# Kernel tuning notes

Hardware: AMD Instinct MI355X
Metric: run time of the kernel (lower is better)

Reference implementation:

```python
import jax, jax.numpy as jnp
import numpy as np

H, D, R, S, K, EV = 8, 256, 6, 2, 2, 2   # num_heads, head_dim, ratio, shared_head, topk, expand_v
HID = 2048
DV = D * EV            # head_v_dim = 512
KEY_DIM = H * D        # 2048
VAL_DIM = KEY_DIM * EV # 4096


def setup_inputs() -> dict:
    key = jax.random.key(0)
    ks = jax.random.split(key, 9)
    b, t = 2, 1024
    def lin(k, fan_in, shape):
        # ~torch default linear init scale
        return jax.random.normal(k, shape, jnp.float32) * (fan_in ** -0.5)
    return {
        "hidden_states": jax.random.normal(ks[0], (b, t, HID), jnp.float32),
        "Wq": lin(ks[1], HID, (HID, KEY_DIM)),
        "Wk": lin(ks[2], HID, (HID, KEY_DIM)),
        "Wv": lin(ks[3], HID, (HID, VAL_DIM)),
        "Wq_exp": lin(ks[4], D, (H, D, D * R)),  # per-head q expert expansion (ModuleList -> batched)
        "Wk_exp": lin(ks[5], D, (H, D, D * R)),
        "Wgate": lin(ks[6], D, (D, R - S)),
        "Wg": lin(ks[7], HID, (HID, VAL_DIM)),
        "Wo": lin(ks[8], VAL_DIM, (VAL_DIM, HID)),
    }


def reference(hidden_states, Wq, Wk, Wv, Wq_exp, Wk_exp, Wgate, Wg, Wo):
    b, t, _ = hidden_states.shape
    # base projections, split into heads: [H, b, t, D]
    q = (hidden_states @ Wq).reshape(b, t, H, D).transpose(2, 0, 1, 3)
    k = (hidden_states @ Wk).reshape(b, t, H, D).transpose(2, 0, 1, 3)
    v = (hidden_states @ Wv).reshape(b, t, H, DV)  # [b, t, H, DV]

    # --- sparse routing on q (gate over ratio - shared experts) ---
    logits = jnp.einsum('hbtd,dn->hbtn', q, Wgate)
    scores = jax.nn.softmax(logits.astype(jnp.float32), axis=-1)
    w, idx = jax.lax.top_k(scores, K)
    w = w / jnp.sum(w, axis=-1, keepdims=True)
    idx = idx + S  # shift past shared experts
    # scatter top-k weights into full [H, b, t, R]
    full = jnp.sum(jax.nn.one_hot(idx, R, dtype=w.dtype) * w[..., None], axis=-2)
    full = full.at[..., :S].set(1.0 / S)
    full = full / jnp.sum(full, axis=-1, keepdims=True)
    rw = full.astype(hidden_states.dtype).transpose(3, 1, 2, 0)  # [R, b, t, H]
    mask = (rw != 0).astype(hidden_states.dtype)                 # [R, b, t, H]

    # --- per-head expert expansions: [R, b, t, H, D] ---
    qe = jnp.einsum('hbtd,hde->hbte', q, Wq_exp).reshape(H, b, t, R, D).transpose(3, 1, 2, 0, 4)
    ke = jnp.einsum('hbtd,hde->hbte', k, Wk_exp).reshape(H, b, t, R, D).transpose(3, 1, 2, 0, 4)
    ve = jnp.broadcast_to(v[None], (R, b, t, H, DV))
    qe = qe * mask[..., None]
    ke = ke * mask[..., None]
    ve = ve * mask[..., None]

    # --- dense attention per (expert, batch, head) ---
    attn = jax.nn.softmax(jnp.einsum('rbqhd,rbkhd->rbhqk', qe, ke) / (D ** 0.5), axis=-1)
    o = jnp.einsum('rbhqk,rbkhd->rbqhd', attn, ve)  # [R, b, t, H, DV]

    # --- weighted combine over experts + gated output ---
    o = jnp.einsum('rbthd,rbth->bthd', o, rw)
    g = (hidden_states @ Wg).reshape(b, t, H, DV)
    o = o * jax.nn.silu(g)
    return o.reshape(b, t, VAL_DIM) @ Wo
```

## Files before the change

kernel.cpp:

```cpp
#include <hip/hip_runtime.h>
#include <hip/hip_bf16.h>
#include <cstdint>
#include <cstddef>

typedef __bf16 bf16_t;
typedef __bf16 bf16x8 __attribute__((ext_vector_type(8)));
typedef float f32x4 __attribute__((ext_vector_type(4)));

typedef __attribute__((address_space(3))) unsigned int lds_uint_t;
typedef __attribute__((address_space(1))) unsigned int glob_uint_t;

__device__ __forceinline__ void gload16(const void* g, void* l) {
  __builtin_amdgcn_global_load_lds((const glob_uint_t*)g, (lds_uint_t*)l, 16, 0, 0);
}

__device__ __forceinline__ f32x4 mfma16(bf16x8 a, bf16x8 b, f32x4 c) {
  return __builtin_amdgcn_mfma_f32_16x16x32_bf16(a, b, c, 0, 0, 0);
}

__global__ __launch_bounds__(256) void conv_bf16_k(const float* __restrict__ in,
                                                   bf16_t* __restrict__ out, int n8) {
  int i = blockIdx.x * 256 + threadIdx.x;
  if (i >= n8) return;
  f32x4 a = *(const f32x4*)(in + (size_t)i * 8);
  f32x4 b = *(const f32x4*)(in + (size_t)i * 8 + 4);
  bf16x8 o;
  o[0] = (bf16_t)a[0]; o[1] = (bf16_t)a[1]; o[2] = (bf16_t)a[2]; o[3] = (bf16_t)a[3];
  o[4] = (bf16_t)b[0]; o[5] = (bf16_t)b[1]; o[6] = (bf16_t)b[2]; o[7] = (bf16_t)b[3];
  *(bf16x8*)(out + (size_t)i * 8) = o;
}

__global__ __launch_bounds__(256) void tconv_k(const float* __restrict__ in, bf16_t* __restrict__ out,
                                               int R, int C, size_t inZ, size_t outZ) {
  __shared__ __align__(16) bf16_t t[64 * 72];
  in += (size_t)blockIdx.z * inZ;
  out += (size_t)blockIdx.z * outZ;
  const int c0 = blockIdx.x * 64, r0 = blockIdx.y * 64;
  const int tid = threadIdx.x;
#pragma unroll
  for (int it = 0; it < 4; it++) {
    int c = tid + it * 256;
    int row = c >> 4, ch = c & 15;
    f32x4 v = *(const f32x4*)(in + (size_t)(r0 + row) * C + c0 + ch * 4);
#pragma unroll
    for (int j = 0; j < 4; j++) t[(ch * 4 + j) * 72 + row] = (bf16_t)v[j];
  }
  __syncthreads();
#pragma unroll
  for (int it = 0; it < 2; it++) {
    int c = tid + it * 256;
    int oc = c >> 3, ch = c & 7;
    bf16x8 v = *(const bf16x8*)(t + oc * 72 + ch * 8);
    *(bf16x8*)(out + (size_t)(c0 + oc) * R + r0 + ch * 8) = v;
  }
}

__global__ __launch_bounds__(256) void tv_k(const bf16_t* __restrict__ v, bf16_t* __restrict__ Vt) {
  __shared__ __align__(16) bf16_t t[64 * 72];
  const int tt0 = blockIdx.x * 64;
  const int dv0 = blockIdx.y * 64;
  const int bh = blockIdx.z;
  const int b = bh >> 3, h = bh & 7;
  const int tid = threadIdx.x;
  const bf16_t* src = v + (size_t)(b * 1024 + tt0) * 12288 + 8192 + h * 512 + dv0;
#pragma unroll
  for (int it = 0; it < 2; it++) {
    int c = tid + it * 256;
    int row = c >> 3, ch = c & 7;
    bf16x8 x = *(const bf16x8*)(src + (size_t)row * 12288 + ch * 8);
#pragma unroll
    for (int j = 0; j < 8; j++) t[(ch * 8 + j) * 72 + row] = x[j];
  }
  __syncthreads();
  bf16_t* dst = Vt + (size_t)bh * 524288 + (size_t)dv0 * 1024 + tt0;
#pragma unroll
  for (int it = 0; it < 2; it++) {
    int c = tid + it * 256;
    int od = c >> 3, ch = c & 7;
    bf16x8 x = *(const bf16x8*)(t + od * 72 + ch * 8);
    *(bf16x8*)(dst + (size_t)od * 1024 + ch * 8) = x;
  }
}

__global__ __launch_bounds__(256) void wfuse_k(const float* __restrict__ Wq, const float* __restrict__ Wgate,
                                               float* __restrict__ Wf) {
  __shared__ float wg[1024];
  const int tid = threadIdx.x;
  for (int i = tid; i < 1024; i += 256) wg[i] = Wgate[i];
  __syncthreads();
  const int kk = blockIdx.x * 64 + (tid & 63);
  const int oid = tid >> 6;
  float acc[8] = {0, 0, 0, 0, 0, 0, 0, 0};
  const float* wr = Wq + (size_t)kk * 2048;
#pragma unroll
  for (int half = 0; half < 2; half++) {
    const int h = oid * 2 + half;
    const float* seg = wr + h * 256;
    for (int d = 0; d < 256; d += 4) {
      f32x4 q4 = *(const f32x4*)(seg + d);
#pragma unroll
      for (int n = 0; n < 4; n++) {
        acc[half * 4 + n] += q4[0] * wg[(d + 0) * 4 + n] + q4[1] * wg[(d + 1) * 4 + n] +
                             q4[2] * wg[(d + 2) * 4 + n] + q4[3] * wg[(d + 3) * 4 + n];
      }
    }
  }
#pragma unroll
  for (int jj = 0; jj < 8; jj++) Wf[(size_t)kk * 32 + oid * 8 + jj] = acc[jj];
}

__global__ __launch_bounds__(256) void logits_k(const float* __restrict__ hs, const float* __restrict__ Wf,
                                                float* __restrict__ lg) {
  __shared__ __align__(16) float hrow[2048];
  __shared__ float red[8][32];
  const int bt = blockIdx.x;
  const int tid = threadIdx.x;
  const float* src = hs + (size_t)bt * 2048;
  for (int i = tid; i < 512; i += 256) *(f32x4*)&hrow[i * 4] = *(const f32x4*)(src + i * 4);
  __syncthreads();
  const int j = tid & 31, part = tid >> 5;
  float acc = 0.f;
  for (int kk = part * 256; kk < part * 256 + 256; kk++) acc += hrow[kk] * Wf[(size_t)kk * 32 + j];
  red[part][j] = acc;
  __syncthreads();
  if (tid < 32) {
    float s = 0.f;
#pragma unroll
    for (int p = 0; p < 8; p++) s += red[p][tid];
    lg[(size_t)bt * 32 + tid] = s;
  }
}

__global__ __launch_bounds__(256) void routing_k(const float* __restrict__ lg, float* __restrict__ rw) {
  int gid = blockIdx.x * 256 + threadIdx.x;
  if (gid >= 16384) return;
  const int h = gid >> 11;
  const int bt = gid & 2047;
  const int b = bt >> 10, tt = bt & 1023;
  f32x4 l = *(const f32x4*)(lg + (size_t)bt * 32 + h * 4);
  float mx = fmaxf(fmaxf(l[0], l[1]), fmaxf(l[2], l[3]));
  float e0 = __expf(l[0] - mx), e1 = __expf(l[1] - mx), e2 = __expf(l[2] - mx), e3 = __expf(l[3] - mx);
  float den = e0 + e1 + e2 + e3;
  float s[4] = {e0 / den, e1 / den, e2 / den, e3 / den};
  int i1 = 0;
#pragma unroll
  for (int i = 1; i < 4; i++) if (s[i] > s[i1]) i1 = i;
  int i2 = (i1 == 0) ? 1 : 0;
#pragma unroll
  for (int i = 0; i < 4; i++) if (i != i1 && s[i] > s[i2]) i2 = i;
  float sw = s[i1] + s[i2];
  float w1 = s[i1] / sw, w2 = s[i2] / sw;
  float tot = 1.0f + w1 + w2;
  float o[6] = {0.5f / tot, 0.5f / tot, 0.f, 0.f, 0.f, 0.f};
  o[2 + i1] = w1 / tot;
  o[2 + i2] = w2 / tot;
#pragma unroll
  for (int r = 0; r < 6; r++) rw[(size_t)((r * 2 + b) * 8 + h) * 1024 + tt] = o[r];
}

__global__ __launch_bounds__(256) void idx_k(const float* __restrict__ rw, int* __restrict__ kidx,
                                             float* __restrict__ maskg, int2* __restrict__ kn) {
  __shared__ int wsum[4];
  const int z = blockIdx.x;
  const int rr = z >> 4, bh = z & 15;
  const int b = bh >> 3, h = bh & 7;
  const float* rwp = rw + (size_t)(((rr + 2) * 2 + b) * 8 + h) * 1024;
  const int tid = threadIdx.x;
  const int lane = tid & 63, wv = tid >> 6;
  int act[4];
  int c = 0;
#pragma unroll
  for (int j = 0; j < 4; j++) { act[j] = (rwp[tid * 4 + j] != 0.f) ? 1 : 0; c += act[j]; }
  int s = c;
  for (int o = 1; o < 64; o <<= 1) { int t = __shfl_up(s, o, 64); if (lane >= o) s += t; }
  if (lane == 63) wsum[wv] = s;
  __syncthreads();
  int base = 0;
  for (int wi = 0; wi < wv; wi++) base += wsum[wi];
  int excl = base + s - c;
  int Na = wsum[0] + wsum[1] + wsum[2] + wsum[3];
  int* kout = kidx + (size_t)z * 1088;
  float* mout = maskg + (size_t)z * 1088;
  int o = excl;
#pragma unroll
  for (int j = 0; j < 4; j++)
    if (act[j]) { kout[o] = tid * 4 + j; mout[o] = 1.f; o++; }
  for (int i = Na + tid; i < 1088; i += 256) { kout[i] = 0; mout[i] = 0.f; }
  if (tid == 0) kn[z] = make_int2(Na, (Na + 63) & ~63);
}

__global__ __launch_bounds__(256) void vgather_k(const bf16_t* __restrict__ qkg, const int* __restrict__ kidx,
                                                 const int2* __restrict__ kn, bf16_t* __restrict__ Vg) {
  __shared__ __align__(16) bf16_t t[64 * 72];
  __shared__ int idx[64];
  const int z = blockIdx.z;
  const int rr = z >> 4, bh = z & 15;
  const int b = bh >> 3, h = bh & 7;
  int2 k = kn[z];
  const int s0 = blockIdx.x * 64;
  if (s0 >= k.y) return;
  const int dv0 = blockIdx.y * 64;
  const int tid = threadIdx.x;
  if (tid < 64) idx[tid] = kidx[(size_t)z * 1088 + s0 + tid];
  __syncthreads();
  int base = 0;
  for (int r2 = 0; r2 < rr; r2++) base += kn[r2 * 16 + bh].y;
#pragma unroll
  for (int it = 0; it < 2; it++) {
    int cc = tid + it * 256;
    int row = cc >> 3, ch = cc & 7;
    const bf16_t* src = qkg + (size_t)(b * 1024 + idx[row]) * 12288 + 8192 + h * 512 + dv0 + ch * 8;
    bf16x8 x = *(const bf16x8*)src;
#pragma unroll
    for (int j = 0; j < 8; j++) t[(ch * 8 + j) * 72 + row] = x[j];
  }
  __syncthreads();
  bf16_t* dst = Vg + (size_t)(bh * 512 + dv0) * 2304 + base + s0;
#pragma unroll
  for (int it = 0; it < 2; it++) {
    int cc = tid + it * 256;
    int od = cc >> 3, ch = cc & 7;
    bf16x8 x = *(const bf16x8*)(t + od * 72 + ch * 8);
    *(bf16x8*)(dst + (size_t)od * 2304 + ch * 8) = x;
  }
}

template <int MODE>
__global__ __launch_bounds__(256) void gemm_bt(const bf16_t* __restrict__ A, const bf16_t* __restrict__ B,
                                               void* __restrict__ Cp, int K, int lda, int ldb, int ldc) {
  __shared__ __align__(16) bf16_t lsA[128 * 64];
  __shared__ __align__(16) bf16_t lsB[128 * 64];
  const int tid = threadIdx.x;
  const int lane = tid & 63, wv = tid >> 6;
  const int lrow = lane & 15, lgrp = lane >> 4;
  const int wr = wv >> 1, wc = wv & 1;
  const int bn = blockIdx.x * 128, bm = blockIdx.y * 128;

  f32x4 zero = {0.f, 0.f, 0.f, 0.f};
  f32x4 acc[4][4];
#pragma unroll
  for (int i = 0; i < 4; i++)
#pragma unroll
    for (int j = 0; j < 4; j++) acc[i][j] = zero;

  for (int k0 = 0; k0 < K; k0 += 64) {
    __syncthreads();
#pragma unroll
    for (int it = 0; it < 4; it++) {
      int c = tid + it * 256;
      int row = c >> 3, coff = (c & 7) * 16;
      gload16((const char*)A + ((size_t)(bm + row) * lda + k0) * 2 + coff, (char*)lsA + row * 128 + coff);
      gload16((const char*)B + ((size_t)(bn + row) * ldb + k0) * 2 + coff, (char*)lsB + row * 128 + coff);
    }
    __syncthreads();
#pragma unroll
    for (int kk = 0; kk < 2; kk++) {
      bf16x8 af[4], bfr[4];
#pragma unroll
      for (int m4 = 0; m4 < 4; m4++)
        af[m4] = *(const bf16x8*)((const char*)lsA + (wr * 64 + m4 * 16 + lrow) * 128 + kk * 64 + lgrp * 16);
#pragma unroll
      for (int n4 = 0; n4 < 4; n4++)
        bfr[n4] = *(const bf16x8*)((const char*)lsB + (wc * 64 + n4 * 16 + lrow) * 128 + kk * 64 + lgrp * 16);
#pragma unroll
      for (int m4 = 0; m4 < 4; m4++)
#pragma unroll
        for (int n4 = 0; n4 < 4; n4++) acc[m4][n4] = mfma16(af[m4], bfr[n4], acc[m4][n4]);
    }
  }
#pragma unroll
  for (int m4 = 0; m4 < 4; m4++) {
#pragma unroll
    for (int i = 0; i < 4; i++) {
      const int row = bm + wr * 64 + m4 * 16 + lgrp * 4 + i;
#pragma unroll
      for (int n4 = 0; n4 < 4; n4++) {
        const int col = bn + wc * 64 + n4 * 16 + lrow;
        float v = acc[m4][n4][i];
        if constexpr (MODE == 0) {
          ((bf16_t*)Cp)[(size_t)row * ldc + col] = (bf16_t)v;
        } else {
          ((float*)Cp)[(size_t)row * ldc + col] = v;
        }
      }
    }
  }
}

__global__ __launch_bounds__(256) void gemm_n64(const bf16_t* __restrict__ A, const bf16_t* __restrict__ B,
                                                float* __restrict__ C, int K, int lda, int ldb, int ldc) {
  __shared__ __align__(16) bf16_t lsA[128 * 64];
  __shared__ __align__(16) bf16_t lsB[64 * 64];
  const int tid = threadIdx.x;
  const int lane = tid & 63, wr = tid >> 6;
  const int lrow = lane & 15, lgrp = lane >> 4;
  const int bn = blockIdx.x * 64, bm = blockIdx.y * 128;

  f32x4 zero = {0.f, 0.f, 0.f, 0.f};
  f32x4 acc[2][4];
#pragma unroll
  for (int i = 0; i < 2; i++)
#pragma unroll
    for (int j = 0; j < 4; j++) acc[i][j] = zero;

  for (int k0 = 0; k0 < K; k0 += 64) {
    __syncthreads();
#pragma unroll
    for (int it = 0; it < 4; it++) {
      int c = tid + it * 256;
      int row = c >> 3, coff = (c & 7) * 16;
      gload16((const char*)A + ((size_t)(bm + row) * lda + k0) * 2 + coff, (char*)lsA + row * 128 + coff);
    }
#pragma unroll
    for (int it = 0; it < 2; it++) {
      int c = tid + it * 256;
      int row = c >> 3, coff = (c & 7) * 16;
      gload16((const char*)B + ((size_t)(bn + row) * ldb + k0) * 2 + coff, (char*)lsB + row * 128 + coff);
    }
    __syncthreads();
#pragma unroll
    for (int kk = 0; kk < 2; kk++) {
      bf16x8 af[2], bfr[4];
#pragma unroll
      for (int m2 = 0; m2 < 2; m2++)
        af[m2] = *(const bf16x8*)((const char*)lsA + (wr * 32 + m2 * 16 + lrow) * 128 + kk * 64 + lgrp * 16);
#pragma unroll
      for (int n4 = 0; n4 < 4; n4++)
        bfr[n4] = *(const bf16x8*)((const char*)lsB + (n4 * 16 + lrow) * 128 + kk * 64 + lgrp * 16);
#pragma unroll
      for (int m2 = 0; m2 < 2; m2++)
#pragma unroll
        for (int n4 = 0; n4 < 4; n4++) acc[m2][n4] = mfma16(af[m2], bfr[n4], acc[m2][n4]);
    }
  }
#pragma unroll
  for (int m2 = 0; m2 < 2; m2++) {
#pragma unroll
    for (int i = 0; i < 4; i++) {
      const int row = bm + wr * 32 + m2 * 16 + lgrp * 4 + i;
#pragma unroll
      for (int n4 = 0; n4 < 4; n4++) {
        C[(size_t)row * ldc + bn + n4 * 16 + lrow] = acc[m2][n4][i];
      }
    }
  }
}

__global__ __launch_bounds__(256) void gemm_exp(const bf16_t* __restrict__ qkg, const bf16_t* __restrict__ Wqe,
                                                const bf16_t* __restrict__ Wke, bf16_t* __restrict__ qeB,
                                                bf16_t* __restrict__ keB) {
  __shared__ __align__(16) bf16_t lsA[128 * 64];
  __shared__ __align__(16) bf16_t lsB[128 * 64];
  const int tid = threadIdx.x;
  const int lane = tid & 63, wv = tid >> 6;
  const int lrow = lane & 15, lgrp = lane >> 4;
  const int wr = wv >> 1, wc = wv & 1;
  const int bn = blockIdx.x * 128, bm = blockIdx.y * 128;
  const int z = blockIdx.z;
  const int sel = z >> 3, hh = z & 7;
  const bf16_t* A = qkg + sel * 2048 + hh * 256;
  const bf16_t* B = (sel ? Wke : Wqe) + (size_t)hh * 393216;
  bf16_t* C = sel ? keB : qeB;

  f32x4 zero = {0.f, 0.f, 0.f, 0.f};
  f32x4 acc[4][4];
#pragma unroll
  for (int i = 0; i < 4; i++)
#pragma unroll
    for (int j = 0; j < 4; j++) acc[i][j] = zero;

  for (int k0 = 0; k0 < 256; k0 += 64) {
    __syncthreads();
#pragma unroll
    for (int it = 0; it < 4; it++) {
      int c = tid + it * 256;
      int row = c >> 3, coff = (c & 7) * 16;
      gload16((const char*)A + ((size_t)(bm + row) * 12288 + k0) * 2 + coff, (char*)lsA + row * 128 + coff);
      gload16((const char*)B + ((size_t)(bn + row) * 256 + k0) * 2 + coff, (char*)lsB + row * 128 + coff);
    }
    __syncthreads();
#pragma unroll
    for (int kk = 0; kk < 2; kk++) {
      bf16x8 af[4], bfr[4];
#pragma unroll
      for (int m4 = 0; m4 < 4; m4++)
        af[m4] = *(const bf16x8*)((const char*)lsA + (wr * 64 + m4 * 16 + lrow) * 128 + kk * 64 + lgrp * 16);
#pragma unroll
      for (int n4 = 0; n4 < 4; n4++)
        bfr[n4] = *(const bf16x8*)((const char*)lsB + (wc * 64 + n4 * 16 + lrow) * 128 + kk * 64 + lgrp * 16);
#pragma unroll
      for (int m4 = 0; m4 < 4; m4++)
#pragma unroll
        for (int n4 = 0; n4 < 4; n4++) acc[m4][n4] = mfma16(af[m4], bfr[n4], acc[m4][n4]);
    }
  }
#pragma unroll
  for (int m4 = 0; m4 < 4; m4++) {
#pragma unroll
    for (int i = 0; i < 4; i++) {
      const int row = bm + wr * 64 + m4 * 16 + lgrp * 4 + i;
      const int bb = row >> 10, tt = row & 1023;
#pragma unroll
      for (int n4 = 0; n4 < 4; n4++) {
        const int col = bn + wc * 64 + n4 * 16 + lrow;
        const int rr = col >> 8, dd = col & 255;
        C[((size_t)((rr * 2 + bb) * 8 + hh) * 1024 + tt) * 256 + dd] = (bf16_t)acc[m4][n4][i];
      }
    }
  }
}

__global__ __launch_bounds__(256, 2) void attn_k(const bf16_t* __restrict__ qe, const bf16_t* __restrict__ ke,
                                                 const bf16_t* __restrict__ Vt, const float* __restrict__ rw,
                                                 const bf16_t* __restrict__ g, bf16_t* __restrict__ oc,
                                                 const int* __restrict__ kidx, const float* __restrict__ maskg,
                                                 const int2* __restrict__ kn, const bf16_t* __restrict__ Vg) {
  __shared__ __align__(16) bf16_t ldsK[2][32 * 256];
  __shared__ __align__(16) bf16_t ldsV[2][256 * 32];
  __shared__ __align__(16) bf16_t ldsP[4 * 16 * 40];
  __shared__ int ldsIdx[1088];

  const int f = (blockIdx.x & 7) * 64 + (blockIdx.x >> 3);
  const int qt = f & 15, dvh = (f >> 4) & 1, bh = f >> 5;

  const int tid = threadIdx.x;
  const int wv = tid >> 6, lane = tid & 63;
  const int lrow = lane & 15, lgrp = lane >> 4;
  const int b = bh >> 3, h = bh & 7;
  const int qw = qt * 64 + wv * 16;

  const char* vtb = (const char*)Vt + ((size_t)bh * 524288 + (size_t)dvh * 262144) * 2;

  f32x4 zero = {0.f, 0.f, 0.f, 0.f};
  f32x4 Otot[16];
#pragma unroll
  for (int n = 0; n < 16; n++) Otot[n] = zero;

  int cur = 0;
  for (int r = 0; r < 6; r++) {
    const size_t rbh = (size_t)((r * 2 + b) * 8 + h);
    const bf16_t* qbase = qe + rbh * 262144;
    const float* rwb = rw + rbh * 1024;
    const char* kbr = (const char*)ke + rbh * 524288;

    int nkt = 32;
    float lpinit = 0.f;
    const float* mgp = nullptr;
    const char* vgb = vtb;
    size_t vstride = 2048;
    const bool routed = (r >= 2);
    if (routed) {
      const int rr = r - 2;
      int2 kkn = kn[rr * 16 + bh];
      nkt = kkn.y >> 5;
      lpinit = (float)(1024 - kkn.x) * 0.0625f;
      int basep = 0;
      for (int r2 = 0; r2 < rr; r2++) basep += kn[r2 * 16 + bh].y;
      vgb = (const char*)Vg + ((size_t)(bh * 512 + dvh * 256) * 2304 + basep) * 2;
      vstride = 4608;
      mgp = maskg + (size_t)(rr * 16 + bh) * 1088;
      __syncthreads();
      const int* kp = kidx + (size_t)(rr * 16 + bh) * 1088;
      for (int i = tid; i < 1088; i += 256) ldsIdx[i] = kp[i];
      __syncthreads();
    }
    if (nkt == 0) continue;

    bf16x8 qf[8];
#pragma unroll
    for (int c = 0; c < 8; c++)
      qf[c] = *(const bf16x8*)(qbase + (size_t)(qw + lrow) * 256 + c * 32 + lgrp * 8);
    float rwq[4];
#pragma unroll
    for (int i = 0; i < 4; i++) rwq[i] = rwb[qw + lgrp * 4 + i];

    float Lp[4] = {lpinit, lpinit, lpinit, lpinit};
    f32x4 accO[16];
#pragma unroll
    for (int n = 0; n < 16; n++) accO[n] = zero;

    auto issue_tile = [&](int kt, int buf) {
      char* lk = (char*)ldsK[buf];
      if (!routed) {
#pragma unroll
        for (int it = 0; it < 4; it++) {
          int p = (wv * 4 + it) * 1024 + (lane << 4);
          int row = p >> 9, off = p & 511;
          gload16(kbr + (size_t)(kt * 32 + row) * 512 + (off ^ ((row & 7) << 4)), lk + p);
        }
      } else {
#pragma unroll
        for (int it = 0; it < 4; it++) {
          int p = (wv * 4 + it) * 1024 + (lane << 4);
          int row = p >> 9, off = p & 511;
          int iv = ldsIdx[kt * 32 + row];
          gload16(kbr + (size_t)iv * 512 + (off ^ ((row & 7) << 4)), lk + p);
        }
      }
      char* lv = (char*)ldsV[buf];
      const char* vb = vgb + (size_t)kt * 64;
#pragma unroll
      for (int it = 0; it < 4; it++) {
        int p = (wv * 4 + it) * 1024 + (lane << 4);
        int row = p >> 6, off = p & 63;
        gload16(vb + (size_t)row * vstride + (off ^ (((row >> 1) & 3) << 4)), lv + p);
      }
    };

    issue_tile(0, cur);
    for (int kt = 0; kt < nkt; kt++) {
      asm volatile("s_waitcnt vmcnt(0) lgkmcnt(0)" ::: "memory");
      __syncthreads();
      if (kt + 1 < nkt) issue_tile(kt + 1, cur ^ 1);
      const char* lK = (const char*)ldsK[cur];
      const char* lV = (const char*)ldsV[cur];
      float mg0 = 1.f, mg1 = 1.f;
      if (routed) { mg0 = mgp[kt * 32 + lrow]; mg1 = mgp[kt * 32 + 16 + lrow]; }

      f32x4 sac0 = zero, sac1 = zero;
      __builtin_amdgcn_s_setprio(1);
#pragma unroll
      for (int c = 0; c < 8; c++) {
        int col = (c * 64 + lgrp * 16) ^ ((lrow & 7) << 4);
        bf16x8 k0 = *(const bf16x8*)(lK + (size_t)lrow * 512 + col);
        bf16x8 k1 = *(const bf16x8*)(lK + (size_t)(16 + lrow) * 512 + col);
        sac0 = mfma16(qf[c], k0, sac0);
        sac1 = mfma16(qf[c], k1, sac1);
      }
      __builtin_amdgcn_s_setprio(0);
      bf16_t* pb = ldsP + wv * 640;
#pragma unroll
      for (int i = 0; i < 4; i++) {
        float p0 = mg0 * __expf(sac0[i] * 0.0625f);
        float p1 = mg1 * __expf(sac1[i] * 0.0625f);
        pb[(i * 4 + lgrp) * 40 + lrow] = (bf16_t)p0;
        pb[(i * 4 + lgrp) * 40 + 16 + lrow] = (bf16_t)p1;
        Lp[i] += p0 + p1;
      }
      bf16x8 pa = *(const bf16x8*)(pb + ((lrow & 3) * 4 + (lrow >> 2)) * 40 + lgrp * 8);
      __builtin_amdgcn_s_setprio(1);
#pragma unroll
      for (int n = 0; n < 16; n++) {
        int row = n * 16 + lrow;
        int col = (lgrp * 16) ^ (((row >> 1) & 3) << 4);
        bf16x8 vf = *(const bf16x8*)(lV + (size_t)row * 64 + col);
        accO[n] = mfma16(pa, vf, accO[n]);
      }
      __builtin_amdgcn_s_setprio(0);
      cur ^= 1;
    }
#pragma unroll
    for (int i = 0; i < 4; i++) {
      float v = Lp[i];
      v += __shfl_xor(v, 1, 16);
      v += __shfl_xor(v, 2, 16);
      v += __shfl_xor(v, 4, 16);
      v += __shfl_xor(v, 8, 16);
      float inv = rwq[i] / v;
#pragma unroll
      for (int n = 0; n < 16; n++) Otot[n][i] += accO[n][i] * inv;
    }
  }

#pragma unroll
  for (int i = 0; i < 4; i++) {
    const size_t grow = ((size_t)(b * 1024 + qw + lgrp * 4 + i)) * 12288 + 4096 + h * 512 + dvh * 256;
    const size_t orow = ((size_t)(b * 1024 + qw + lgrp * 4 + i)) * 4096 + h * 512 + dvh * 256;
#pragma unroll
    for (int n = 0; n < 16; n++) {
      float gv = (float)g[grow + n * 16 + lrow];
      float sg = gv / (1.f + __expf(-gv));
      oc[orow + n * 16 + lrow] = (bf16_t)(Otot[n][i] * sg);
    }
  }
}

extern "C" void kernel_launch(void* const* d_in, const int* in_sizes, int n_in,
                              void* d_out, int out_size, void* d_ws, size_t ws_size,
                              hipStream_t stream) {
  const float* hs  = (const float*)d_in[0];
  const float* Wq  = (const float*)d_in[1];
  const float* Wk  = (const float*)d_in[2];
  const float* Wv  = (const float*)d_in[3];
  const float* Wqe = (const float*)d_in[4];
  const float* Wke = (const float*)d_in[5];
  const float* Wgt = (const float*)d_in[6];
  const float* Wg  = (const float*)d_in[7];
  const float* Wo  = (const float*)d_in[8];
  float* out = (float*)d_out;

  const size_t MB = 1024 * 1024;
  char* w = (char*)d_ws;
  bf16_t* hs_bf = (bf16_t*)(w + 0 * MB);
  bf16_t* WcatT = (bf16_t*)(w + 8 * MB);
  bf16_t* qeB   = (bf16_t*)(w + 0 * MB);
  bf16_t* WoT   = (bf16_t*)(w + 56 * MB);
  bf16_t* WqeT  = (bf16_t*)(w + 72 * MB);
  bf16_t* WkeT  = (bf16_t*)(w + 78 * MB);
  bf16_t* qkg   = (bf16_t*)(w + 84 * MB);
  bf16_t* Vt    = (bf16_t*)(w + 132 * MB);
  bf16_t* keB   = (bf16_t*)(w + 148 * MB);
  bf16_t* ocB   = (bf16_t*)(w + 196 * MB);
  float*  Wf    = (float*)(w + 212 * MB);
  float*  lg    = (float*)(w + 212 * MB + 262144);
  float*  rwB   = (float*)(w + 212 * MB + 524288);
  bf16_t* VgB   = (bf16_t*)(w + 214 * MB);
  int*    kidxB = (int*)(w + 250 * MB);
  float*  maskgB= (float*)(w + 250 * MB + 524288);
  int2*   knB   = (int2*)(w + 250 * MB + 1048576);
  (void)ws_size; (void)in_sizes; (void)n_in; (void)out_size;

  conv_bf16_k<<<2048, 256, 0, stream>>>(hs, hs_bf, 524288);
  tconv_k<<<dim3(32, 32, 1), 256, 0, stream>>>(Wq, WcatT, 2048, 2048, 0, 0);
  tconv_k<<<dim3(32, 32, 1), 256, 0, stream>>>(Wk, WcatT + 2048 * 2048, 2048, 2048, 0, 0);
  tconv_k<<<dim3(64, 32, 1), 256, 0, stream>>>(Wg, WcatT + 4096 * 2048, 2048, 4096, 0, 0);
  tconv_k<<<dim3(64, 32, 1), 256, 0, stream>>>(Wv, WcatT + 8192 * 2048, 2048, 4096, 0, 0);
  tconv_k<<<dim3(32, 64, 1), 256, 0, stream>>>(Wo, WoT, 4096, 2048, 0, 0);
  tconv_k<<<dim3(24, 4, 8), 256, 0, stream>>>(Wqe, WqeT, 256, 1536, 393216, 393216);
  tconv_k<<<dim3(24, 4, 8), 256, 0, stream>>>(Wke, WkeT, 256, 1536, 393216, 393216);

  wfuse_k<<<32, 256, 0, stream>>>(Wq, Wgt, Wf);
  logits_k<<<2048, 256, 0, stream>>>(hs, Wf, lg);
  routing_k<<<64, 256, 0, stream>>>(lg, rwB);
  idx_k<<<64, 256, 0, stream>>>(rwB, kidxB, maskgB, knB);

  gemm_bt<0><<<dim3(96, 16, 1), 256, 0, stream>>>(hs_bf, WcatT, qkg, 2048, 2048, 2048, 12288);
  tv_k<<<dim3(16, 8, 16), 256, 0, stream>>>(qkg, Vt);
  vgather_k<<<dim3(16, 8, 64), 256, 0, stream>>>(qkg, kidxB, knB, VgB);

  gemm_exp<<<dim3(12, 16, 16), 256, 0, stream>>>(qkg, WqeT, WkeT, qeB, keB);

  attn_k<<<512, 256, 0, stream>>>(qeB, keB, Vt, rwB, qkg, ocB, kidxB, maskgB, knB, VgB);

  gemm_n64<<<dim3(32, 16, 1), 256, 0, stream>>>(ocB, WoT, out, 4096, 4096, 4096, 2048);
}
```

Before: 701.0 us.

## Compute routed key expansions only for selected tokens via gathered GEMM

The key-expert GEMM now covers only the two shared experts over all tokens. A new gathered GEMM computes routed-expert key expansions only for tokens each (expert, batch, head) selected, and writes them contiguously. The attention kernel then loads routed K tiles sequentially instead of through an LDS index table, which removes the index staging and its barriers. This cuts the FLOPs and bytes for unused routed keys, at the cost of one extra launch and scattered row gathers on the A side.

```diff
diff --git a/kernel.cpp b/kernel.cpp
--- a/kernel.cpp
+++ b/kernel.cpp
@@ -349,6 +349,9 @@
 __global__ __launch_bounds__(256) void gemm_exp(const bf16_t* __restrict__ qkg, const bf16_t* __restrict__ Wqe,
                                                 const bf16_t* __restrict__ Wke, bf16_t* __restrict__ qeB,
                                                 bf16_t* __restrict__ keB) {
+  const int z = blockIdx.z;
+  const int sel = z >> 3, hh = z & 7;
+  if (sel == 1 && blockIdx.x >= 4) return;
   __shared__ __align__(16) bf16_t lsA[128 * 64];
   __shared__ __align__(16) bf16_t lsB[128 * 64];
   const int tid = threadIdx.x;
@@ -356,8 +359,6 @@
   const int lrow = lane & 15, lgrp = lane >> 4;
   const int wr = wv >> 1, wc = wv & 1;
   const int bn = blockIdx.x * 128, bm = blockIdx.y * 128;
-  const int z = blockIdx.z;
-  const int sel = z >> 3, hh = z & 7;
   const bf16_t* A = qkg + sel * 2048 + hh * 256;
   const bf16_t* B = (sel ? Wke : Wqe) + (size_t)hh * 393216;
   bf16_t* C = sel ? keB : qeB;
@@ -410,15 +411,82 @@
   }
 }
 
+__global__ __launch_bounds__(256) void gemm_kg(const bf16_t* __restrict__ qkg, const bf16_t* __restrict__ Wke,
+                                               const int* __restrict__ kidx, const int2* __restrict__ kn,
+                                               bf16_t* __restrict__ keG) {
+  const int z = blockIdx.z;
+  const int rr = z >> 4, bh = z & 15;
+  const int bm = blockIdx.y * 128;
+  if (bm >= kn[z].y) return;
+  __shared__ __align__(16) bf16_t lsA[128 * 64];
+  __shared__ __align__(16) bf16_t lsB[128 * 64];
+  __shared__ int sidx[128];
+  const int b = bh >> 3, h = bh & 7;
+  const int bn = blockIdx.x * 128;
+  const int tid = threadIdx.x;
+  const int lane = tid & 63, wv = tid >> 6;
+  const int lrow = lane & 15, lgrp = lane >> 4;
+  const int wr = wv >> 1, wc = wv & 1;
+  if (tid < 128) sidx[tid] = kidx[(size_t)z * 1088 + bm + tid];
+  const bf16_t* Abase = qkg + 2048 + h * 256;
+  const bf16_t* B = Wke + (size_t)h * 393216 + (size_t)((rr + 2) * 256 + bn) * 256;
+
+  f32x4 zero = {0.f, 0.f, 0.f, 0.f};
+  f32x4 acc[4][4];
+#pragma unroll
+  for (int i = 0; i < 4; i++)
+#pragma unroll
+    for (int j = 0; j < 4; j++) acc[i][j] = zero;
+
+  for (int k0 = 0; k0 < 256; k0 += 64) {
+    __syncthreads();
+#pragma unroll
+    for (int it = 0; it < 4; it++) {
+      int c = tid + it * 256;
+      int row = c >> 3, coff = (c & 7) * 16;
+      gload16((const char*)(Abase + ((size_t)(b * 1024 + sidx[row]) * 12288 + k0)) + coff,
+              (char*)lsA + row * 128 + coff);
+      gload16((const char*)B + ((size_t)row * 256 + k0) * 2 + coff, (char*)lsB + row * 128 + coff);
+    }
+    __syncthreads();
+#pragma unroll
+    for (int kk = 0; kk < 2; kk++) {
+      bf16x8 af[4], bfr[4];
+#pragma unroll
+      for (int m4 = 0; m4 < 4; m4++)
+        af[m4] = *(const bf16x8*)((const char*)lsA + (wr * 64 + m4 * 16 + lrow) * 128 + kk * 64 + lgrp * 16);
+#pragma unroll
+      for (int n4 = 0; n4 < 4; n4++)
+        bfr[n4] = *(const bf16x8*)((const char*)lsB + (wc * 64 + n4 * 16 + lrow) * 128 + kk * 64 + lgrp * 16);
+#pragma unroll
+      for (int m4 = 0; m4 < 4; m4++)
+#pragma unroll
+        for (int n4 = 0; n4 < 4; n4++) acc[m4][n4] = mfma16(af[m4], bfr[n4], acc[m4][n4]);
+    }
+  }
+#pragma unroll
+  for (int m4 = 0; m4 < 4; m4++) {
+#pragma unroll
+    for (int i = 0; i < 4; i++) {
+      const int row = bm + wr * 64 + m4 * 16 + lgrp * 4 + i;
+#pragma unroll
+      for (int n4 = 0; n4 < 4; n4++) {
+        const int col = bn + wc * 64 + n4 * 16 + lrow;
+        keG[((size_t)z * 1088 + row) * 256 + col] = (bf16_t)acc[m4][n4][i];
+      }
+    }
+  }
+}
+
+
 __global__ __launch_bounds__(256, 2) void attn_k(const bf16_t* __restrict__ qe, const bf16_t* __restrict__ ke,
-                                                 const bf16_t* __restrict__ Vt, const float* __restrict__ rw,
-                                                 const bf16_t* __restrict__ g, bf16_t* __restrict__ oc,
-                                                 const int* __restrict__ kidx, const float* __restrict__ maskg,
+                                                 const bf16_t* __restrict__ keG, const bf16_t* __restrict__ Vt,
+                                                 const float* __restrict__ rw, const bf16_t* __restrict__ g,
+                                                 bf16_t* __restrict__ oc, const float* __restrict__ maskg,
                                                  const int2* __restrict__ kn, const bf16_t* __restrict__ Vg) {
   __shared__ __align__(16) bf16_t ldsK[2][32 * 256];
   __shared__ __align__(16) bf16_t ldsV[2][256 * 32];
   __shared__ __align__(16) bf16_t ldsP[4 * 16 * 40];
-  __shared__ int ldsIdx[1088];
 
   const int f = (blockIdx.x & 7) * 64 + (blockIdx.x >> 3);
   const int qt = f & 15, dvh = (f >> 4) & 1, bh = f >> 5;
@@ -441,13 +509,13 @@
     const size_t rbh = (size_t)((r * 2 + b) * 8 + h);
     const bf16_t* qbase = qe + rbh * 262144;
     const float* rwb = rw + rbh * 1024;
-    const char* kbr = (const char*)ke + rbh * 524288;
 
     int nkt = 32;
     float lpinit = 0.f;
     const float* mgp = nullptr;
     const char* vgb = vtb;
     size_t vstride = 2048;
+    const char* kbase = (const char*)ke + rbh * 524288;
     const bool routed = (r >= 2);
     if (routed) {
       const int rr = r - 2;
@@ -459,10 +527,7 @@
       vgb = (const char*)Vg + ((size_t)(bh * 512 + dvh * 256) * 2304 + basep) * 2;
       vstride = 4608;
       mgp = maskg + (size_t)(rr * 16 + bh) * 1088;
-      __syncthreads();
-      const int* kp = kidx + (size_t)(rr * 16 + bh) * 1088;
-      for (int i = tid; i < 1088; i += 256) ldsIdx[i] = kp[i];
-      __syncthreads();
+      kbase = (const char*)keG + (size_t)(rr * 16 + bh) * 557056;
     }
     if (nkt == 0) continue;
 
@@ -481,21 +546,11 @@
 
     auto issue_tile = [&](int kt, int buf) {
       char* lk = (char*)ldsK[buf];
-      if (!routed) {
-#pragma unroll
-        for (int it = 0; it < 4; it++) {
-          int p = (wv * 4 + it) * 1024 + (lane << 4);
-          int row = p >> 9, off = p & 511;
-          gload16(kbr + (size_t)(kt * 32 + row) * 512 + (off ^ ((row & 7) << 4)), lk + p);
-        }
-      } else {
-#pragma unroll
-        for (int it = 0; it < 4; it++) {
-          int p = (wv * 4 + it) * 1024 + (lane << 4);
-          int row = p >> 9, off = p & 511;
-          int iv = ldsIdx[kt * 32 + row];
-          gload16(kbr + (size_t)iv * 512 + (off ^ ((row & 7) << 4)), lk + p);
-        }
+#pragma unroll
+      for (int it = 0; it < 4; it++) {
+        int p = (wv * 4 + it) * 1024 + (lane << 4);
+        int row = p >> 9, off = p & 511;
+        gload16(kbase + (size_t)(kt * 32 + row) * 512 + (off ^ ((row & 7) << 4)), lk + p);
       }
       char* lv = (char*)ldsV[buf];
       const char* vb = vgb + (size_t)kt * 64;
@@ -600,14 +655,15 @@
   bf16_t* qkg   = (bf16_t*)(w + 84 * MB);
   bf16_t* Vt    = (bf16_t*)(w + 132 * MB);
   bf16_t* keB   = (bf16_t*)(w + 148 * MB);
-  bf16_t* ocB   = (bf16_t*)(w + 196 * MB);
-  float*  Wf    = (float*)(w + 212 * MB);
-  float*  lg    = (float*)(w + 212 * MB + 262144);
-  float*  rwB   = (float*)(w + 212 * MB + 524288);
+  bf16_t* keG   = (bf16_t*)(w + 164 * MB);
+  bf16_t* ocB   = (bf16_t*)(w + 198 * MB);
   bf16_t* VgB   = (bf16_t*)(w + 214 * MB);
-  int*    kidxB = (int*)(w + 250 * MB);
-  float*  maskgB= (float*)(w + 250 * MB + 524288);
-  int2*   knB   = (int2*)(w + 250 * MB + 1048576);
+  float*  Wf    = (float*)(w + 250 * MB);
+  float*  lg    = (float*)(w + 250 * MB + 262144);
+  float*  rwB   = (float*)(w + 250 * MB + 524288);
+  int*    kidxB = (int*)(w + 251 * MB);
+  float*  maskgB= (float*)(w + 251 * MB + 524288);
+  int2*   knB   = (int2*)(w + 251 * MB + 1048576);
   (void)ws_size; (void)in_sizes; (void)n_in; (void)out_size;
 
   conv_bf16_k<<<2048, 256, 0, stream>>>(hs, hs_bf, 524288);
@@ -629,8 +685,9 @@
   vgather_k<<<dim3(16, 8, 64), 256, 0, stream>>>(qkg, kidxB, knB, VgB);
 
   gemm_exp<<<dim3(12, 16, 16), 256, 0, stream>>>(qkg, WqeT, WkeT, qeB, keB);
-
-  attn_k<<<512, 256, 0, stream>>>(qeB, keB, Vt, rwB, qkg, ocB, kidxB, maskgB, knB, VgB);
+  gemm_kg<<<dim3(2, 8, 64), 256, 0, stream>>>(qkg, WkeT, kidxB, knB, keG);
+
+  attn_k<<<512, 256, 0, stream>>>(qeB, keB, keG, Vt, rwB, qkg, ocB, maskgB, knB, VgB);
 
   gemm_n64<<<dim3(32, 16, 1), 256, 0, stream>>>(ocB, WoT, out, 4096, 4096, 4096, 2048);
 }
```

Result: faster. 668.8 us (-4.6%).
